# Kernel tuning notes

Measured on AMD Instinct MI355X. Metric: run time of the kernel, lower is better.

Reference implementation:

```python
import jax, jax.numpy as jnp
import numpy as np

D_MODEL = 1024
N_HEADS = 16
HEAD_DIM = D_MODEL // N_HEADS


def setup_inputs() -> dict:
    key = jax.random.key(0)
    k_x, k_wqkv, k_bqkv, k_wo, k_bo = jax.random.split(key, 5)
    B, T = 2, 2048
    scale = 1.0 / np.sqrt(D_MODEL)
    return {
        "x": jax.random.normal(k_x, (B, T, D_MODEL), dtype=jnp.float32),
        "W_qkv": jax.random.normal(k_wqkv, (D_MODEL, 3 * D_MODEL), dtype=jnp.float32) * scale,
        "b_qkv": jax.random.normal(k_bqkv, (3 * D_MODEL,), dtype=jnp.float32) * 0.01,
        "W_out": jax.random.normal(k_wo, (D_MODEL, D_MODEL), dtype=jnp.float32) * scale,
        "b_out": jax.random.normal(k_bo, (D_MODEL,), dtype=jnp.float32) * 0.01,
    }


def reference(x, W_qkv, b_qkv, W_out, b_out):
    B, T, C = x.shape
    qkv = x @ W_qkv + b_qkv                      # [B,T,3C]
    q, k, v = jnp.split(qkv, 3, axis=-1)
    def heads(t):
        return t.reshape(B, T, N_HEADS, HEAD_DIM).transpose(0, 2, 1, 3)  # [B,H,T,d]
    q, k, v = heads(q), heads(k), heads(v)
    att = jnp.einsum('bhqd,bhkd->bhqk', q, k) / np.sqrt(HEAD_DIM)
    causal = jnp.tril(jnp.ones((T, T), dtype=bool))
    att = jnp.where(causal, att, -jnp.inf)
    att = jax.nn.softmax(att, axis=-1)
    out = jnp.einsum('bhqk,bhkd->bhqd', att, v)  # [B,H,T,d]
    out = out.transpose(0, 2, 1, 3).reshape(B, T, C)
    return out @ W_out + b_out
```

## Files before the change

kernel.cpp:

```cpp
#include <hip/hip_runtime.h>
#include <hip/hip_bf16.h>
#include <math.h>

typedef __bf16 bf16;
typedef __attribute__((ext_vector_type(8))) __bf16 bf16x8;
typedef __attribute__((ext_vector_type(4))) __bf16 bf16x4;
typedef __attribute__((ext_vector_type(4))) float f32x4;
typedef __attribute__((ext_vector_type(16))) float f32x16;
typedef __attribute__((ext_vector_type(4))) unsigned u32x4;

#define T_SEQ 2048

static __device__ __forceinline__ float fast_exp2(float x) {
#if __has_builtin(__builtin_amdgcn_exp2f)
    return __builtin_amdgcn_exp2f(x);
#else
    return __expf(x * 0.69314718f);
#endif
}

static __device__ __forceinline__ unsigned pk(float lo, float hi) {
    unsigned a = (unsigned)__builtin_bit_cast(unsigned short, (bf16)lo);
    unsigned b = (unsigned)__builtin_bit_cast(unsigned short, (bf16)hi);
    return a | (b << 16);
}

static __device__ __forceinline__ void gload_lds16(const bf16* g, bf16* l) {
    __builtin_amdgcn_global_load_lds((const __attribute__((address_space(1))) void*)g,
                                     (__attribute__((address_space(3))) void*)l, 16, 0, 0);
}

static __device__ __forceinline__ int swz(int row, int colb) {
    return row * 128 + (colb ^ ((row & 7) << 4));
}

__global__ void convert_kernel(const float* __restrict__ x, bf16* __restrict__ xb, int n4)
{
    int i = blockIdx.x * blockDim.x + threadIdx.x;
    int stride = gridDim.x * blockDim.x;
    for (; i < n4; i += stride) {
        f32x4 v = ((const f32x4*)x)[i];
        bf16x4 o;
        o[0] = (bf16)v[0]; o[1] = (bf16)v[1]; o[2] = (bf16)v[2]; o[3] = (bf16)v[3];
        ((bf16x4*)xb)[i] = o;
    }
}

__global__ __launch_bounds__(256) void transpose_conv_kernel(
    const float* __restrict__ W, bf16* __restrict__ Wt, int K, int N)
{
    __shared__ float tile[32][33];
    int tx = threadIdx.x & 31, ty = threadIdx.x >> 5;
    int n0 = blockIdx.x * 32, k0 = blockIdx.y * 32;
#pragma unroll
    for (int j = 0; j < 4; ++j)
        tile[ty + j * 8][tx] = W[(size_t)(k0 + ty + j * 8) * N + n0 + tx];
    __syncthreads();
#pragma unroll
    for (int j = 0; j < 4; ++j)
        Wt[(size_t)(n0 + ty + j * 8) * K + k0 + tx] = (bf16)tile[tx][ty + j * 8];
}

template<int BM, int BN, int BLK, int WGN, int VMODE>
__global__ __launch_bounds__(BLK, 2) void gemm2ph_kernel(
    const bf16* __restrict__ A, const bf16* __restrict__ Bt,
    const float* __restrict__ bias, void* __restrict__ Cout,
    bf16* __restrict__ Vtout, int M, int N, int K, int GX)
{
    constexpr int WAVES = BLK / 64, WGM = WAVES / WGN;
    constexpr int MR = BM / (WGM * 16), NR = BN / (WGN * 16);
    constexpr int A_RND = BM * 8 / BLK, B_RND = BN * 8 / BLK;
    constexpr int LDS_HALF = (BM + BN) * 128;
    __shared__ __align__(16) char lds[2 * LDS_HALF];

    const int tid = threadIdx.x, lane = tid & 63, wid = tid >> 6;
    const int wm = wid / WGN, wn = wid % WGN;
    const int l15 = lane & 15, l4 = lane >> 4;
    const int cpx = gridDim.x >> 3;
    const int sbid = ((int)blockIdx.x & 7) * cpx + ((int)blockIdx.x >> 3);
    const int m0 = (sbid / GX) * BM, n0 = (sbid % GX) * BN;
    const int wu = tid & ~63;

    f32x4 acc[MR][NR] = {};
    const int NT = K >> 6;

    auto stage = [&](int b, int kt) {
        char* Ab = lds + b * LDS_HALF;
        char* Bb = Ab + BM * 128;
#pragma unroll
        for (int j = 0; j < A_RND; ++j) {
            int ch = j * BLK + tid, r = ch >> 3;
            int c = ((ch & 7) ^ (r & 7)) * 8;
            gload_lds16(&A[(size_t)(m0 + r) * K + kt + c],
                        (bf16*)Ab + (size_t)(j * BLK + wu) * 8);
        }
#pragma unroll
        for (int j = 0; j < B_RND; ++j) {
            int ch = j * BLK + tid, r = ch >> 3;
            int c = ((ch & 7) ^ (r & 7)) * 8;
            gload_lds16(&Bt[(size_t)(n0 + r) * K + kt + c],
                        (bf16*)Bb + (size_t)(j * BLK + wu) * 8);
        }
    };

    stage(0, 0);
    asm volatile("s_waitcnt vmcnt(0)" ::: "memory");
    __builtin_amdgcn_s_barrier();

    for (int t = 0; t < NT; ++t) {
        if (t + 1 < NT) stage((t + 1) & 1, (t + 1) * 64);
        const char* Ab = lds + (t & 1) * LDS_HALF;
        const char* Bb = Ab + BM * 128;
#pragma unroll
        for (int kk = 0; kk < 2; ++kk) {
            bf16x8 af[MR], bfr[NR];
#pragma unroll
            for (int mi = 0; mi < MR; ++mi) {
                int row = wm * (MR * 16) + mi * 16 + l15;
                af[mi] = *(const bf16x8*)(Ab + swz(row, kk * 64 + l4 * 16));
            }
#pragma unroll
            for (int ni = 0; ni < NR; ++ni) {
                int row = wn * (NR * 16) + ni * 16 + l15;
                bfr[ni] = *(const bf16x8*)(Bb + swz(row, kk * 64 + l4 * 16));
            }
#pragma unroll
            for (int mi = 0; mi < MR; ++mi)
#pragma unroll
                for (int ni = 0; ni < NR; ++ni)
                    acc[mi][ni] = __builtin_amdgcn_mfma_f32_16x16x32_bf16(
                        af[mi], bfr[ni], acc[mi][ni], 0, 0, 0);
        }
        asm volatile("s_waitcnt vmcnt(0)" ::: "memory");
        __builtin_amdgcn_s_barrier();
    }

#pragma unroll
    for (int ni = 0; ni < NR; ++ni) {
        const int colb = n0 + wn * (NR * 16) + ni * 16;
        const int col = colb + l15;
        float bv = bias[col];
        if (VMODE == 2 && colb >= 2048) {
            bf16* wtile = (bf16*)lds + wid * (16 * 72);
#pragma unroll
            for (int mi = 0; mi < MR; ++mi)
#pragma unroll
                for (int r = 0; r < 4; ++r)
                    wtile[l15 * 72 + mi * 16 + l4 * 4 + r] = (bf16)(acc[mi][ni][r] + bv);
            asm volatile("s_waitcnt lgkmcnt(0)" ::: "memory");
            const int hd_l = lane >> 2, tc = lane & 3;
            bf16x8 c0 = *(const bf16x8*)&wtile[hd_l * 72 + tc * 16];
            bf16x8 c1 = *(const bf16x8*)&wtile[hd_l * 72 + tc * 16 + 8];
            asm volatile("s_waitcnt lgkmcnt(0)" ::: "memory");
            const int row0 = m0 + wm * (MR * 16);
            const int bb = row0 >> 11, t0g = row0 & (T_SEQ - 1);
            bf16* dst = &Vtout[((size_t)(bb * 1024 + (colb - 2048) + hd_l)) * T_SEQ + t0g + tc * 16];
            *(bf16x8*)dst = c0;
            *(bf16x8*)(dst + 8) = c1;
        } else {
#pragma unroll
            for (int mi = 0; mi < MR; ++mi)
#pragma unroll
                for (int r = 0; r < 4; ++r) {
                    int row = m0 + wm * (MR * 16) + mi * 16 + l4 * 4 + r;
                    float v = acc[mi][ni][r] + bv;
                    if (VMODE) ((bf16*)Cout)[(size_t)row * N + col] = (bf16)v;
                    else       ((float*)Cout)[(size_t)row * N + col] = v;
                }
        }
    }
}

__global__ __launch_bounds__(256, 3) void attn_kernel(
    const bf16* __restrict__ qkv, const bf16* __restrict__ Vt, bf16* __restrict__ attb)
{
    __shared__ __align__(16) char smem[32768];
    const int tid = threadIdx.x, lane = tid & 63, wid = tid >> 6;
    const int qg = wid >> 1, par = wid & 1;
    const int bid = blockIdx.x;
    const int iq = 31 - (bid >> 5);
    const int bh = bid & 31, b = bh >> 4, h = bh & 15;
    const int nt = iq + 1, npairs = (nt + 1) >> 1;
    const int l31 = lane & 31, hi = lane >> 5, hib = hi * 16;
    const size_t base = (size_t)b * T_SEQ * 3072;
    const int koff = 1024 + h * 64;
    const size_t vtb = (size_t)bh * 64 * T_SEQ;
    const int sr = tid >> 2, sq4 = tid & 3;

    const int q0 = iq * 64 + qg * 32;
    const int qrow = q0 + l31;

    bf16x8 Qf[4];
#pragma unroll
    for (int ds = 0; ds < 4; ++ds)
        Qf[ds] = *(const bf16x8*)&qkv[base + (size_t)qrow * 3072 + h * 64 + ds * 16 + hi * 8];

    bf16x8 onesA;
#pragma unroll
    for (int j = 0; j < 8; ++j) onesA[j] = (bf16)1.0f;

    f32x16 Oacc[2] = {};
    f32x16 lacc = {};

    bf16x8 kreg[2][2], vreg[2][2];
    {
#pragma unroll
        for (int p = 0; p < 2; ++p)
#pragma unroll
            for (int j = 0; j < 2; ++j) {
                kreg[p][j] = *(const bf16x8*)&qkv[base + (size_t)(p * 64 + sr) * 3072
                                                 + koff + sq4 * 16 + j * 8];
                vreg[p][j] = *(const bf16x8*)&Vt[vtb + (size_t)sr * T_SEQ + p * 64 + sq4 * 16 + j * 8];
            }
    }

    for (int u = 0; u < npairs; ++u) {
        __syncthreads();
#pragma unroll
        for (int p = 0; p < 2; ++p) {
            char* Kp = smem + p * 8192;
            char* Vp = smem + 16384 + p * 8192;
#pragma unroll
            for (int j = 0; j < 2; ++j) {
                const int byte = swz(sr, sq4 * 32 + j * 16);
                *(bf16x8*)(Kp + byte) = kreg[p][j];
                *(bf16x8*)(Vp + byte) = vreg[p][j];
            }
        }
        __syncthreads();
        if (u + 1 < npairs) {
            const int pb = (u + 1) * 128;
#pragma unroll
            for (int p = 0; p < 2; ++p)
#pragma unroll
                for (int j = 0; j < 2; ++j) {
                    kreg[p][j] = *(const bf16x8*)&qkv[base + (size_t)(pb + p * 64 + sr) * 3072
                                                     + koff + sq4 * 16 + j * 8];
                    vreg[p][j] = *(const bf16x8*)&Vt[vtb + (size_t)sr * T_SEQ + pb + p * 64 + sq4 * 16 + j * 8];
                }
        }
        const int t = 2 * u + par;
        if (t < nt) {
            const char* Kc = smem + par * 8192;
            const char* Vc = smem + 16384 + par * 8192;
            f32x16 S[2] = {};
            __builtin_amdgcn_s_setprio(1);
#pragma unroll
            for (int ds = 0; ds < 4; ++ds)
#pragma unroll
                for (int kt = 0; kt < 2; ++kt) {
                    bf16x8 af = *(const bf16x8*)(Kc + swz(kt * 32 + l31, ds * 32 + hib));
                    S[kt] = __builtin_amdgcn_mfma_f32_32x32x16_bf16(af, Qf[ds], S[kt], 0, 0, 0);
                }
            __builtin_amdgcn_s_setprio(0);
            if (t == nt - 1) {
                const int qloc = qg * 32 + l31;
#pragma unroll
                for (int kt = 0; kt < 2; ++kt)
#pragma unroll
                    for (int j = 0; j < 16; ++j) {
                        const int kloc = kt * 32 + (j & 3) + 8 * (j >> 2) + 4 * hi;
                        if (kloc > qloc) S[kt][j] = -3.0e38f;
                    }
            }
#pragma unroll
            for (int kt = 0; kt < 2; ++kt)
#pragma unroll
                for (int j = 0; j < 16; ++j)
                    S[kt][j] = fast_exp2(S[kt][j] * 0.18033688f);
            __builtin_amdgcn_s_setprio(1);
#pragma unroll
            for (int ks = 0; ks < 4; ++ks) {
                const int kt = ks >> 1, bs = (ks & 1) * 8;
                unsigned P01 = pk(S[kt][bs + 0], S[kt][bs + 1]);
                unsigned P23 = pk(S[kt][bs + 2], S[kt][bs + 3]);
                unsigned P45 = pk(S[kt][bs + 4], S[kt][bs + 5]);
                unsigned P67 = pk(S[kt][bs + 6], S[kt][bs + 7]);
                auto r02 = __builtin_amdgcn_permlane32_swap(P01, P45, false, false);
                auto r13 = __builtin_amdgcn_permlane32_swap(P23, P67, false, false);
                u32x4 wv;
                wv[0] = r02[0]; wv[1] = r13[0]; wv[2] = r02[1]; wv[3] = r13[1];
                bf16x8 Bfrag = __builtin_bit_cast(bf16x8, wv);
#pragma unroll
                for (int dt = 0; dt < 2; ++dt) {
                    bf16x8 av = *(const bf16x8*)(Vc + swz(dt * 32 + l31, ks * 32 + hib));
                    Oacc[dt] = __builtin_amdgcn_mfma_f32_32x32x16_bf16(av, Bfrag, Oacc[dt], 0, 0, 0);
                }
                lacc = __builtin_amdgcn_mfma_f32_32x32x16_bf16(onesA, Bfrag, lacc, 0, 0, 0);
            }
            __builtin_amdgcn_s_setprio(0);
        }
    }

    float* cbuf = (float*)smem;
    __syncthreads();
    if (par == 1) {
        float* p = cbuf + (qg * 64 + lane) * 36;
#pragma unroll
        for (int dt = 0; dt < 2; ++dt)
#pragma unroll
            for (int j = 0; j < 16; ++j) p[dt * 16 + j] = Oacc[dt][j];
        p[32] = lacc[0];
    }
    __syncthreads();
    if (par == 0) {
        const float* p = cbuf + (qg * 64 + lane) * 36;
        float inv = 1.f / (lacc[0] + p[32]);
#pragma unroll
        for (int dt = 0; dt < 2; ++dt) {
#pragma unroll
            for (int g = 0; g < 4; ++g) {
                bf16x4 o;
#pragma unroll
                for (int j = 0; j < 4; ++j)
                    o[j] = (bf16)((Oacc[dt][g * 4 + j] + p[dt * 16 + g * 4 + j]) * inv);
                const int d = dt * 32 + g * 8 + 4 * hi;
                *(bf16x4*)&attb[((size_t)b * T_SEQ + qrow) * 1024 + h * 64 + d] = o;
            }
        }
    }
}

extern "C" void kernel_launch(void* const* d_in, const int* in_sizes, int n_in,
                              void* d_out, int out_size, void* d_ws, size_t ws_size,
                              hipStream_t stream)
{
    const float* x    = (const float*)d_in[0];
    const float* Wqkv = (const float*)d_in[1];
    const float* bqkv = (const float*)d_in[2];
    const float* Wout = (const float*)d_in[3];
    const float* bout = (const float*)d_in[4];
    float* out = (float*)d_out;

    char* ws = (char*)d_ws;
    bf16* xb    = (bf16*)(ws);
    bf16* Wqkvt = (bf16*)(ws + (8ull  << 20));
    bf16* Woutt = (bf16*)(ws + (14ull << 20));
    bf16* qkvb  = (bf16*)(ws + (16ull << 20));
    bf16* attb  = (bf16*)(ws + (40ull << 20));
    bf16* Vt    = (bf16*)(ws + (48ull << 20));

    convert_kernel<<<dim3(2048), dim3(256), 0, stream>>>(x, xb, (4096 * 1024) / 4);
    transpose_conv_kernel<<<dim3(96, 32), dim3(256), 0, stream>>>(Wqkv, Wqkvt, 1024, 3072);
    transpose_conv_kernel<<<dim3(32, 32), dim3(256), 0, stream>>>(Wout, Woutt, 1024, 1024);
    gemm2ph_kernel<128, 192, 256, 2, 2><<<dim3(512), dim3(256), 0, stream>>>(
        xb, Wqkvt, bqkv, (void*)qkvb, Vt, 4096, 3072, 1024, 16);
    attn_kernel<<<dim3(1024), dim3(256), 0, stream>>>(qkvb, Vt, attb);
    gemm2ph_kernel<128, 64, 256, 2, 0><<<dim3(512), dim3(256), 0, stream>>>(
        attb, Woutt, bout, (void*)out, nullptr, 4096, 1024, 1024, 16);
}
```

Before: 91.30 us.

## Use triple-buffered 512-thread GEMM with MFMA priority for QKV projection

The QKV projection GEMM becomes a new kernel with three LDS stages, so loads are issued two tiles ahead and each iteration waits only on the older tile via a partial vmcnt. Blocks grow to 512 threads (8 waves, 4 along N), which halves per-wave tile work. s_setprio is raised around the MFMA block. The output GEMM keeps the old double-buffered kernel, now without the V-transpose path. The costs are more LDS per block, an occupancy hint of one block, and a hardcoded vmcnt value that only holds for this tile config.

```diff
diff --git a/kernel.cpp b/kernel.cpp
--- a/kernel.cpp
+++ b/kernel.cpp
@@ -62,7 +62,7 @@
 }
 
 template<int BM, int BN, int BLK, int WGN, int VMODE>
-__global__ __launch_bounds__(BLK, 2) void gemm2ph_kernel(
+__global__ __launch_bounds__(BLK, 1) void gemm3s_kernel(
     const bf16* __restrict__ A, const bf16* __restrict__ Bt,
     const float* __restrict__ bias, void* __restrict__ Cout,
     bf16* __restrict__ Vtout, int M, int N, int K, int GX)
@@ -70,8 +70,9 @@
     constexpr int WAVES = BLK / 64, WGM = WAVES / WGN;
     constexpr int MR = BM / (WGM * 16), NR = BN / (WGN * 16);
     constexpr int A_RND = BM * 8 / BLK, B_RND = BN * 8 / BLK;
-    constexpr int LDS_HALF = (BM + BN) * 128;
-    __shared__ __align__(16) char lds[2 * LDS_HALF];
+    static_assert(A_RND + B_RND == 5, "vmcnt immediate hardcoded to 5");
+    constexpr int LDS_TILE = (BM + BN) * 128;
+    __shared__ __align__(16) char lds[3 * LDS_TILE];
 
     const int tid = threadIdx.x, lane = tid & 63, wid = tid >> 6;
     const int wm = wid / WGN, wn = wid % WGN;
@@ -85,7 +86,7 @@
     const int NT = K >> 6;
 
     auto stage = [&](int b, int kt) {
-        char* Ab = lds + b * LDS_HALF;
+        char* Ab = lds + b * LDS_TILE;
         char* Bb = Ab + BM * 128;
 #pragma unroll
         for (int j = 0; j < A_RND; ++j) {
@@ -104,12 +105,14 @@
     };
 
     stage(0, 0);
-    asm volatile("s_waitcnt vmcnt(0)" ::: "memory");
-    __builtin_amdgcn_s_barrier();
+    stage(1, 64);
 
     for (int t = 0; t < NT; ++t) {
-        if (t + 1 < NT) stage((t + 1) & 1, (t + 1) * 64);
-        const char* Ab = lds + (t & 1) * LDS_HALF;
+        if (t + 1 < NT) asm volatile("s_waitcnt vmcnt(5)" ::: "memory");
+        else            asm volatile("s_waitcnt vmcnt(0)" ::: "memory");
+        __builtin_amdgcn_s_barrier();
+        if (t + 2 < NT) stage((t + 2) % 3, (t + 2) * 64);
+        const char* Ab = lds + (t % 3) * LDS_TILE;
         const char* Bb = Ab + BM * 128;
 #pragma unroll
         for (int kk = 0; kk < 2; ++kk) {
@@ -124,17 +127,18 @@
                 int row = wn * (NR * 16) + ni * 16 + l15;
                 bfr[ni] = *(const bf16x8*)(Bb + swz(row, kk * 64 + l4 * 16));
             }
+            __builtin_amdgcn_s_setprio(1);
 #pragma unroll
             for (int mi = 0; mi < MR; ++mi)
 #pragma unroll
                 for (int ni = 0; ni < NR; ++ni)
                     acc[mi][ni] = __builtin_amdgcn_mfma_f32_16x16x32_bf16(
                         af[mi], bfr[ni], acc[mi][ni], 0, 0, 0);
-        }
-        asm volatile("s_waitcnt vmcnt(0)" ::: "memory");
-        __builtin_amdgcn_s_barrier();
-    }
-
+            __builtin_amdgcn_s_setprio(0);
+        }
+    }
+
+    __syncthreads();
 #pragma unroll
     for (int ni = 0; ni < NR; ++ni) {
         const int colb = n0 + wn * (NR * 16) + ni * 16;
@@ -171,6 +175,97 @@
     }
 }
 
+template<int BM, int BN, int BLK, int WGN, int OUT_BF16>
+__global__ __launch_bounds__(BLK, 2) void gemm2ph_kernel(
+    const bf16* __restrict__ A, const bf16* __restrict__ Bt,
+    const float* __restrict__ bias, void* __restrict__ Cout,
+    int M, int N, int K, int GX)
+{
+    constexpr int WAVES = BLK / 64, WGM = WAVES / WGN;
+    constexpr int MR = BM / (WGM * 16), NR = BN / (WGN * 16);
+    constexpr int A_RND = BM * 8 / BLK, B_RND = BN * 8 / BLK;
+    constexpr int LDS_HALF = (BM + BN) * 128;
+    __shared__ __align__(16) char lds[2 * LDS_HALF];
+
+    const int tid = threadIdx.x, lane = tid & 63, wid = tid >> 6;
+    const int wm = wid / WGN, wn = wid % WGN;
+    const int l15 = lane & 15, l4 = lane >> 4;
+    const int cpx = gridDim.x >> 3;
+    const int sbid = ((int)blockIdx.x & 7) * cpx + ((int)blockIdx.x >> 3);
+    const int m0 = (sbid / GX) * BM, n0 = (sbid % GX) * BN;
+    const int wu = tid & ~63;
+
+    f32x4 acc[MR][NR] = {};
+    const int NT = K >> 6;
+
+    auto stage = [&](int b, int kt) {
+        char* Ab = lds + b * LDS_HALF;
+        char* Bb = Ab + BM * 128;
+#pragma unroll
+        for (int j = 0; j < A_RND; ++j) {
+            int ch = j * BLK + tid, r = ch >> 3;
+            int c = ((ch & 7) ^ (r & 7)) * 8;
+            gload_lds16(&A[(size_t)(m0 + r) * K + kt + c],
+                        (bf16*)Ab + (size_t)(j * BLK + wu) * 8);
+        }
+#pragma unroll
+        for (int j = 0; j < B_RND; ++j) {
+            int ch = j * BLK + tid, r = ch >> 3;
+            int c = ((ch & 7) ^ (r & 7)) * 8;
+            gload_lds16(&Bt[(size_t)(n0 + r) * K + kt + c],
+                        (bf16*)Bb + (size_t)(j * BLK + wu) * 8);
+        }
+    };
+
+    stage(0, 0);
+    asm volatile("s_waitcnt vmcnt(0)" ::: "memory");
+    __builtin_amdgcn_s_barrier();
+
+    for (int t = 0; t < NT; ++t) {
+        if (t + 1 < NT) stage((t + 1) & 1, (t + 1) * 64);
+        const char* Ab = lds + (t & 1) * LDS_HALF;
+        const char* Bb = Ab + BM * 128;
+#pragma unroll
+        for (int kk = 0; kk < 2; ++kk) {
+            bf16x8 af[MR], bfr[NR];
+#pragma unroll
+            for (int mi = 0; mi < MR; ++mi) {
+                int row = wm * (MR * 16) + mi * 16 + l15;
+                af[mi] = *(const bf16x8*)(Ab + swz(row, kk * 64 + l4 * 16));
+            }
+#pragma unroll
+            for (int ni = 0; ni < NR; ++ni) {
+                int row = wn * (NR * 16) + ni * 16 + l15;
+                bfr[ni] = *(const bf16x8*)(Bb + swz(row, kk * 64 + l4 * 16));
+            }
+#pragma unroll
+            for (int mi = 0; mi < MR; ++mi)
+#pragma unroll
+                for (int ni = 0; ni < NR; ++ni)
+                    acc[mi][ni] = __builtin_amdgcn_mfma_f32_16x16x32_bf16(
+                        af[mi], bfr[ni], acc[mi][ni], 0, 0, 0);
+        }
+        asm volatile("s_waitcnt vmcnt(0)" ::: "memory");
+        __builtin_amdgcn_s_barrier();
+    }
+
+#pragma unroll
+    for (int mi = 0; mi < MR; ++mi) {
+#pragma unroll
+        for (int ni = 0; ni < NR; ++ni) {
+            int col = n0 + wn * (NR * 16) + ni * 16 + l15;
+            float bv = bias[col];
+#pragma unroll
+            for (int r = 0; r < 4; ++r) {
+                int row = m0 + wm * (MR * 16) + mi * 16 + l4 * 4 + r;
+                float v = acc[mi][ni][r] + bv;
+                if (OUT_BF16) ((bf16*)Cout)[(size_t)row * N + col] = (bf16)v;
+                else          ((float*)Cout)[(size_t)row * N + col] = v;
+            }
+        }
+    }
+}
+
 __global__ __launch_bounds__(256, 3) void attn_kernel(
     const bf16* __restrict__ qkv, const bf16* __restrict__ Vt, bf16* __restrict__ attb)
 {
@@ -343,9 +438,9 @@
     convert_kernel<<<dim3(2048), dim3(256), 0, stream>>>(x, xb, (4096 * 1024) / 4);
     transpose_conv_kernel<<<dim3(96, 32), dim3(256), 0, stream>>>(Wqkv, Wqkvt, 1024, 3072);
     transpose_conv_kernel<<<dim3(32, 32), dim3(256), 0, stream>>>(Wout, Woutt, 1024, 1024);
-    gemm2ph_kernel<128, 192, 256, 2, 2><<<dim3(512), dim3(256), 0, stream>>>(
+    gemm3s_kernel<128, 192, 512, 4, 2><<<dim3(512), dim3(512), 0, stream>>>(
         xb, Wqkvt, bqkv, (void*)qkvb, Vt, 4096, 3072, 1024, 16);
     attn_kernel<<<dim3(1024), dim3(256), 0, stream>>>(qkvb, Vt, attb);
     gemm2ph_kernel<128, 64, 256, 2, 0><<<dim3(512), dim3(256), 0, stream>>>(
-        attb, Woutt, bout, (void*)out, nullptr, 4096, 1024, 1024, 16);
-}
+        attb, Woutt, bout, (void*)out, 4096, 1024, 1024, 16);
+}
```

Result: slower. 99.53 us (+9.0%).
